# Optimization experiments

Hardware: AMD Instinct MI355X
Metric: run time of the kernel (lower is better)

The kernel has to match this reference:

```python
import jax, jax.numpy as jnp
import numpy as np

V, H, B, T = 32000, 1024, 32, 256  # vocab, rnn_size, batch, seq_length


def setup_inputs() -> dict:
    key = jax.random.key(0)
    ks = jax.random.split(key, 6)
    s = 1.0 / np.sqrt(H)
    return {
        "input_data": jax.random.randint(ks[0], (B, T), 0, V, dtype=jnp.int32),
        "targets": jax.random.randint(ks[1], (B, T), 0, V, dtype=jnp.int32),
        "embedding": jax.random.uniform(ks[2], (V, H), minval=-1.0, maxval=1.0, dtype=jnp.float32),
        "softmax_b": jnp.zeros((V,), jnp.float32),
        "W0": (jax.random.normal(ks[3], (2 * H, 4 * H)) * s).astype(jnp.float32),
        "b0": jnp.zeros((4 * H,), jnp.float32),
        "W1": (jax.random.normal(ks[4], (2 * H, 4 * H)) * s).astype(jnp.float32),
        "b1": jnp.zeros((4 * H,), jnp.float32),
    }


def _lstm_step(x, c, h, W, b):
    # TF LSTMCell: gates i, j, f, o; forget_bias = 1.0
    z = jnp.concatenate([x, h], axis=-1) @ W + b  # [B, 4H]
    i, j, f, o = jnp.split(z, 4, axis=-1)
    c2 = c * jax.nn.sigmoid(f + 1.0) + jax.nn.sigmoid(i) * jnp.tanh(j)
    h2 = jax.nn.sigmoid(o) * jnp.tanh(c2)
    return c2, h2


def reference(input_data, targets, embedding, softmax_b, W0, b0, W1, b1):
    x = embedding[input_data]  # [B, T, H]
    Bb, Hh = x.shape[0], embedding.shape[1]
    zeros = jnp.zeros((Bb, Hh), x.dtype)
    init = ((zeros, zeros), (zeros, zeros))  # ((c0,h0),(c1,h1))

    def step(carry, xt):
        (c0, h0), (c1, h1) = carry
        c0, h0 = _lstm_step(xt, c0, h0, W0, b0)
        c1, h1 = _lstm_step(h0, c1, h1, W1, b1)
        return ((c0, h0), (c1, h1)), h1

    _, outs = jax.lax.scan(step, init, jnp.swapaxes(x, 0, 1))  # [T, B, H]
    output = jnp.swapaxes(outs, 0, 1).reshape(-1, Hh)  # [B*T, H]
    logits = output @ embedding.T + softmax_b  # tied softmax weights, [B*T, V]
    labels = targets.reshape(-1)
    logp = jax.nn.log_softmax(logits)
    loss = -jnp.take_along_axis(logp, labels[:, None], axis=1)[:, 0]
    cost = jnp.sum(loss) / Bb
    return logits, cost
```

## Files before the change

kernel.cpp:

```cpp
#include <hip/hip_runtime.h>
#include <hip/hip_bf16.h>

#define DEV static __device__ __forceinline__

typedef unsigned short u16;
typedef unsigned long long u64;
typedef __attribute__((ext_vector_type(8))) short short8;
typedef __attribute__((ext_vector_type(4))) float f32x4;

constexpr int V = 32000, H = 1024, B = 32, T = 256;
constexpr int BT = B * T;
constexpr int G  = 4 * H;
constexpr int NCH = V / 256;
constexpr int NWG2 = 256;
constexpr int RSTRIDE = 32 * 2048 + 2048;

constexpr size_t SZ_WT    = (size_t)G * 2048 * 2;
constexpr size_t OFF_W0T  = 0;
constexpr size_t OFF_W1T  = OFF_W0T + SZ_WT;
constexpr size_t OFF_EBF  = OFF_W1T + SZ_WT;
constexpr size_t OFF_XBF  = OFF_EBF + (size_t)V * H * 2;
constexpr size_t OFF_XP0  = OFF_XBF + (size_t)BT * H * 2;
constexpr size_t OFF_H1   = OFF_XP0 + (size_t)BT * G * 2;
constexpr size_t OFF_HSEQ = OFF_H1 + (size_t)BT * H * 2;
constexpr size_t SZ_HSEQ  = (size_t)(T + 2) * RSTRIDE * 2;
constexpr size_t OFF_SYNC = OFF_HSEQ + SZ_HSEQ;
constexpr size_t OFF_PMAX = OFF_SYNC + 8192;
constexpr size_t OFF_PSUM = OFF_PMAX + (size_t)BT * NCH * 4;
constexpr size_t OFF_LOSS = OFF_PSUM + (size_t)BT * NCH * 4;

DEV u16 f2bf(float x) {
  union { float f; unsigned int u; } v; v.f = x;
  unsigned int r = v.u + 0x7fffu + ((v.u >> 16) & 1u);
  return (u16)(r >> 16);
}
DEV float bf2f(u16 b) {
  union { unsigned int u; float f; } v; v.u = ((unsigned int)b) << 16;
  return v.f;
}
DEV float sigm(float x) { return 1.f / (1.f + expf(-x)); }

DEV void gload_lds16(const u16* g, u16* l) {
  __builtin_amdgcn_global_load_lds(
      (__attribute__((address_space(1))) void*)g,
      (__attribute__((address_space(3))) void*)l, 16, 0, 0);
}


__global__ void k_transpose_cvt2(const float* __restrict__ in0, u16* __restrict__ out0,
                                 const float* __restrict__ in1, u16* __restrict__ out1) {
  const float* in = blockIdx.z ? in1 : in0;
  u16* out = blockIdx.z ? out1 : out0;
  __shared__ float tile[32][33];
  int bc = blockIdx.x * 32, br = blockIdx.y * 32;
  int tx = threadIdx.x & 31, ty0 = threadIdx.x >> 5;
#pragma unroll
  for (int i = 0; i < 4; ++i) {
    int ty = ty0 + i * 8;
    tile[ty][tx] = in[(size_t)(br + ty) * G + bc + tx];
  }
  __syncthreads();
#pragma unroll
  for (int i = 0; i < 4; ++i) {
    int ty = ty0 + i * 8;
    out[(size_t)(bc + ty) * 2048 + br + tx] = f2bf(tile[tx][ty]);
  }
}

__global__ void k_cvt_bf16(const float* __restrict__ in, u16* __restrict__ out, int n4) {
  int i = blockIdx.x * blockDim.x + threadIdx.x;
  int stride = gridDim.x * blockDim.x;
  for (; i < n4; i += stride) {
    float4 v = ((const float4*)in)[i];
    ushort4 o;
    o.x = f2bf(v.x); o.y = f2bf(v.y); o.z = f2bf(v.z); o.w = f2bf(v.w);
    ((ushort4*)out)[i] = o;
  }
}

__global__ void k_gather_x(const float* __restrict__ emb, const int* __restrict__ inp,
                           u16* __restrict__ Xbf) {
  int row = blockIdx.x;
  int t = row >> 5, b = row & 31;
  int tok = inp[b * T + t];
  const float4* src = (const float4*)(emb + (size_t)tok * H);
  ushort4* dst = (ushort4*)(Xbf + (size_t)row * H);
  float4 v = src[threadIdx.x];
  ushort4 o;
  o.x = f2bf(v.x); o.y = f2bf(v.y); o.z = f2bf(v.z); o.w = f2bf(v.w);
  dst[threadIdx.x] = o;
}

__global__ void k_zero(unsigned int* __restrict__ p, int nwords) {
  int i = blockIdx.x * blockDim.x + threadIdx.x;
  int stride = gridDim.x * blockDim.x;
  for (; i < nwords; i += stride) p[i] = 0u;
}

constexpr int GNT = 32;

DEV void stage256(const u16* __restrict__ A, int lda,
                  const u16* __restrict__ Bt, int ldb,
                  int row0, int col0, u16* lds, int t, int h, int tid) {
  int op = h >> 1, hh = h & 1;
  int wid = tid >> 6, lane = tid & 63;
  int r = hh * 128 + wid * 16 + (lane >> 2);
  int k = t * 32 + (((lane & 3) ^ ((lane >> 2) & 3)) << 3);
  const u16* g = (op == 0) ? (A + (size_t)(row0 + r) * lda + k)
                           : (Bt + (size_t)(col0 + r) * ldb + k);
  u16* l = lds + (size_t)((op * 3 + (t % 3)) * 8192 + (hh * 128 + wid * 16) * 32);
  gload_lds16(g, l);
}

template <int MODE>
__global__ __launch_bounds__(512)
void k_gemm256(const u16* __restrict__ A, int lda,
               const u16* __restrict__ Bt, int ldb,
               float* __restrict__ C, int ldc,
               const float* __restrict__ bias,
               float* __restrict__ pmax, float* __restrict__ psum, int nch) {
  __shared__ alignas(16) u16 lds[6 * 8192];

  unsigned nwg = gridDim.x * gridDim.y;
  unsigned flat = blockIdx.y * gridDim.x + blockIdx.x;
  unsigned nf = (flat & 7) * (nwg >> 3) + (flat >> 3);
  int bx = nf % gridDim.x, by = nf / gridDim.x;
  int row0 = by * 256, col0 = bx * 256;

  int tid = threadIdx.x, lane = tid & 63, wid = tid >> 6;
  int wr = wid >> 2, wc = wid & 3;
  int c15 = lane & 15, q4 = lane >> 4;
  int usw = (q4 ^ (c15 & 3)) << 3;

  f32x4 acc[8][4];
#pragma unroll
  for (int m = 0; m < 8; ++m)
#pragma unroll
    for (int n = 0; n < 4; ++n) acc[m][n] = (f32x4){0.f, 0.f, 0.f, 0.f};

#pragma unroll
  for (int h = 0; h < 4; ++h) stage256(A, lda, Bt, ldb, row0, col0, lds, 0, h, tid);
#pragma unroll
  for (int h = 0; h < 4; ++h) stage256(A, lda, Bt, ldb, row0, col0, lds, 1, h, tid);
  asm volatile("s_waitcnt vmcnt(4)" ::: "memory");
  __builtin_amdgcn_sched_barrier(0);
  __builtin_amdgcn_s_barrier();

  short8 af[4], bfr[4];

  for (int t = 0; t < GNT; ++t) {
    const u16* la = lds + (size_t)(t % 3) * 8192;
    const u16* lb = lds + (size_t)(3 + t % 3) * 8192;

#pragma unroll
    for (int m = 0; m < 4; ++m)
      af[m] = *(const short8*)(la + (wr * 128 + m * 16 + c15) * 32 + usw);
#pragma unroll
    for (int n = 0; n < 4; ++n)
      bfr[n] = *(const short8*)(lb + (wc * 64 + n * 16 + c15) * 32 + usw);
    if (t + 2 < GNT) {
      stage256(A, lda, Bt, ldb, row0, col0, lds, t + 2, 0, tid);
      stage256(A, lda, Bt, ldb, row0, col0, lds, t + 2, 1, tid);
    }
    __builtin_amdgcn_s_barrier();
    asm volatile("s_waitcnt lgkmcnt(0)" ::: "memory");
    __builtin_amdgcn_sched_barrier(0);
    __builtin_amdgcn_s_setprio(1);
#pragma unroll
    for (int m = 0; m < 4; ++m)
#pragma unroll
      for (int n = 0; n < 4; ++n)
        acc[m][n] = __builtin_amdgcn_mfma_f32_16x16x32_bf16(af[m], bfr[n], acc[m][n], 0, 0, 0);
    __builtin_amdgcn_s_setprio(0);
    __builtin_amdgcn_s_barrier();

#pragma unroll
    for (int m = 0; m < 4; ++m)
      af[m] = *(const short8*)(la + (wr * 128 + (m + 4) * 16 + c15) * 32 + usw);
    if (t + 2 < GNT) {
      stage256(A, lda, Bt, ldb, row0, col0, lds, t + 2, 2, tid);
      stage256(A, lda, Bt, ldb, row0, col0, lds, t + 2, 3, tid);
    }
    __builtin_amdgcn_s_barrier();
    asm volatile("s_waitcnt lgkmcnt(0)" ::: "memory");
    __builtin_amdgcn_sched_barrier(0);
    __builtin_amdgcn_s_setprio(1);
#pragma unroll
    for (int m = 0; m < 4; ++m)
#pragma unroll
      for (int n = 0; n < 4; ++n)
        acc[m + 4][n] = __builtin_amdgcn_mfma_f32_16x16x32_bf16(af[m], bfr[n], acc[m + 4][n], 0, 0, 0);
    __builtin_amdgcn_s_setprio(0);
    if (t < GNT - 2) {
      asm volatile("s_waitcnt vmcnt(4)" ::: "memory");
      __builtin_amdgcn_sched_barrier(0);
    } else if (t == GNT - 2) {
      asm volatile("s_waitcnt vmcnt(0)" ::: "memory");
      __builtin_amdgcn_sched_barrier(0);
    }
    __builtin_amdgcn_s_barrier();
  }

  float bias_n[4];
#pragma unroll
  for (int n = 0; n < 4; ++n) bias_n[n] = bias[col0 + wc * 64 + n * 16 + c15];

  float2* red = (float2*)lds;
  __syncthreads();

#pragma unroll
  for (int m = 0; m < 8; ++m) {
#pragma unroll
    for (int jr = 0; jr < 4; ++jr) {
      int rloc = wr * 128 + m * 16 + q4 * 4 + jr;
      int r_g = row0 + rloc;
      float v[4];
#pragma unroll
      for (int n = 0; n < 4; ++n) {
        int c_g = col0 + wc * 64 + n * 16 + c15;
        float val = acc[m][n][jr] + bias_n[n];
        if (MODE == 1) {
          C[(size_t)r_g * ldc + c_g] = val;
        } else {
          int tt = r_g >> 5, bb = r_g & 31;
          int q = c_g >> 10, wgup = (c_g & 1023) >> 3, uu = c_g & 7;
          ((u16*)C)[((((size_t)tt * 128 + wgup) * 32 + bb) * 32) + q * 8 + uu] = f2bf(val);
        }
        v[n] = val;
      }
      if (MODE == 1) {
        float mx = fmaxf(fmaxf(v[0], v[1]), fmaxf(v[2], v[3]));
        float s = __expf(v[0] - mx) + __expf(v[1] - mx) + __expf(v[2] - mx) + __expf(v[3] - mx);
#pragma unroll
        for (int d = 1; d < 16; d <<= 1) {
          float mo = __shfl_xor(mx, d, 64);
          float so = __shfl_xor(s, d, 64);
          float M2 = fmaxf(mx, mo);
          s = s * __expf(mx - M2) + so * __expf(mo - M2);
          mx = M2;
        }
        if (c15 == 0) red[rloc * 4 + wc] = make_float2(mx, s);
      }
    }
  }
  if (MODE == 1) {
    __syncthreads();
    if (tid < 256) {
      float M = -1e30f, S = 0.f;
#pragma unroll
      for (int i = 0; i < 4; ++i) {
        float2 a = red[tid * 4 + i];
        float M2 = fmaxf(M, a.x);
        S = S * __expf(M - M2) + a.y * __expf(a.x - M2);
        M = M2;
      }
      pmax[(size_t)(row0 + tid) * nch + bx] = M;
      psum[(size_t)(row0 + tid) * nch + bx] = S;
    }
  }
}


#define RED(w_, bt_, nt_, r_, c_) red[((((w_)*2 + (bt_)) * 2 + (nt_)) * 16 + (r_)) * 16 + (c_)]

DEV void grid_barrier(int* __restrict__ sync, int wg, int gen) {
  __syncthreads();
  if (threadIdx.x == 0) {
    int g = wg >> 4;
    int old = __hip_atomic_fetch_add(sync + g * 64, 1,
                                     __ATOMIC_RELAXED, __HIP_MEMORY_SCOPE_AGENT);
    if (old == 16 * gen - 1) {
      int m = __hip_atomic_fetch_add(sync + 16 * 64, 1,
                                     __ATOMIC_RELAXED, __HIP_MEMORY_SCOPE_AGENT);
      if (m == 16 * gen - 1)
        __hip_atomic_store(sync + 17 * 64, gen,
                           __ATOMIC_RELAXED, __HIP_MEMORY_SCOPE_AGENT);
    }
    while (__hip_atomic_load(sync + 17 * 64,
                             __ATOMIC_RELAXED, __HIP_MEMORY_SCOPE_AGENT) < gen)
      __builtin_amdgcn_s_sleep(2);
  }
  __builtin_amdgcn_sched_barrier(0);
  __syncthreads();
}

template <int KH, bool IS_L0>
DEV void lstm_role(const u16* __restrict__ WT,
                   const u16* __restrict__ xp0p,
                   const float* __restrict__ zb1,
                   u16* __restrict__ hseq, u16* __restrict__ H1bf,
                   int* __restrict__ sync,
                   float* __restrict__ red, int wgu, int wg) {
  constexpr int KOFF = IS_L0 ? 1024 : 0;
  constexpr int KS = KH / 4;
  constexpr int NKC = KS / 32;
  int tid = threadIdx.x, lane = tid & 63, w = tid >> 6;
  int c15 = lane & 15, q4 = lane >> 4;
  int eb = tid >> 3, eu = tid & 7;

  short8 wfr[2][NKC];
#pragma unroll
  for (int nt = 0; nt < 2; ++nt) {
    int lr = nt * 16 + c15;
    const u16* rp = WT + (size_t)((lr >> 3) * 1024 + wgu * 8 + (lr & 7)) * 2048
                    + KOFF + w * KS + q4 * 8;
#pragma unroll
    for (int kc = 0; kc < NKC; ++kc)
      wfr[nt][kc] = *(const short8*)(rp + kc * 32);
  }

  float zpc[4];
  if (!IS_L0) {
#pragma unroll
    for (int q = 0; q < 4; ++q) zpc[q] = zb1[q * 1024 + wgu * 8 + eu];
  }
  float creg = 0.f;

  for (int tick = 0; tick <= T; ++tick) {
    if (IS_L0 ? (tick < T) : (tick >= 1)) {
      int t = tick;
      float zp[4];
      if (IS_L0) {
#pragma unroll
        for (int q = 0; q < 4; ++q)
          zp[q] = bf2f(xp0p[((((size_t)t * 128 + wgu) * 32 + eb) * 32) + q * 8 + eu]);
      } else {
#pragma unroll
        for (int q = 0; q < 4; ++q) zp[q] = zpc[q];
      }

      const u16* hread = hseq + (size_t)t * RSTRIDE;
      f32x4 acc[2][2];
#pragma unroll
      for (int bt = 0; bt < 2; ++bt)
#pragma unroll
        for (int nt = 0; nt < 2; ++nt) acc[bt][nt] = (f32x4){0.f, 0.f, 0.f, 0.f};

#pragma unroll
      for (int kc = 0; kc < NKC; ++kc) {
        int kh = w * KS + kc * 32 + q4 * 8;
        short8 a0 = *(const short8*)(hread + (size_t)c15 * 2048 + kh);
        short8 a1 = *(const short8*)(hread + (size_t)(16 + c15) * 2048 + kh);
        acc[0][0] = __builtin_amdgcn_mfma_f32_16x16x32_bf16(a0, wfr[0][kc], acc[0][0], 0, 0, 0);
        acc[0][1] = __builtin_amdgcn_mfma_f32_16x16x32_bf16(a0, wfr[1][kc], acc[0][1], 0, 0, 0);
        acc[1][0] = __builtin_amdgcn_mfma_f32_16x16x32_bf16(a1, wfr[0][kc], acc[1][0], 0, 0, 0);
        acc[1][1] = __builtin_amdgcn_mfma_f32_16x16x32_bf16(a1, wfr[1][kc], acc[1][1], 0, 0, 0);
      }

#pragma unroll
      for (int bt = 0; bt < 2; ++bt)
#pragma unroll
        for (int nt = 0; nt < 2; ++nt)
#pragma unroll
          for (int jr = 0; jr < 4; ++jr)
            RED(w, bt, nt, q4 * 4 + jr, c15) = acc[bt][nt][jr];
      __syncthreads();

      int bt = eb >> 4, rr = eb & 15;
      float z[4];
#pragma unroll
      for (int q = 0; q < 4; ++q) {
        int lr = q * 8 + eu, nt = lr >> 4, cc = lr & 15;
        z[q] = RED(0, bt, nt, rr, cc) + RED(1, bt, nt, rr, cc) +
               RED(2, bt, nt, rr, cc) + RED(3, bt, nt, rr, cc) + zp[q];
      }
      float gi = sigm(z[0]);
      float gj = tanhf(z[1]);
      float gf = sigm(z[2] + 1.f);
      float go = sigm(z[3]);
      creg = creg * gf + gi * gj;
      float hv = go * tanhf(creg);

      int hb = (int)f2bf(hv);
      int hp = __shfl_xor(hb, 1, 64);
      if (!(tid & 1)) {
        unsigned int pack = (unsigned int)(u16)hb | ((unsigned int)(u16)hp << 16);
        u16* hwr = hseq + (size_t)(t + 1) * RSTRIDE + (IS_L0 ? 0 : 1024);
        __hip_atomic_store((unsigned int*)(hwr + (size_t)eb * 2048 + wgu * 8 + eu), pack,
                           __ATOMIC_RELAXED, __HIP_MEMORY_SCOPE_AGENT);
        if (!IS_L0)
          *(unsigned int*)(H1bf + ((size_t)eb * T + (t - 1)) * H + wgu * 8 + eu) = pack;
      }
    }
    grid_barrier(sync, wg, tick + 1);
  }
}

__global__ __launch_bounds__(256, 1)
void k_lstm_persistent(const u16* __restrict__ W0T, const u16* __restrict__ W1T,
                       const u16* __restrict__ xp0p, const float* __restrict__ b1,
                       u16* __restrict__ hseq, u16* __restrict__ H1bf,
                       int* __restrict__ sync) {
  __shared__ float red[4 * 2 * 2 * 16 * 16];
  int wg = blockIdx.x;
  if (wg < 128)
    lstm_role<1024, true>(W0T, xp0p, nullptr, hseq, H1bf, sync, red, wg, wg);
  else
    lstm_role<2048, false>(W1T, nullptr, b1, hseq, H1bf, sync, red, wg - 128, wg);
}

__global__ void k_rowfin(const float* __restrict__ pmax, const float* __restrict__ psum,
                         const float* __restrict__ Cl, const int* __restrict__ targets,
                         float* __restrict__ loss) {
  int lane = threadIdx.x & 63, wv = threadIdx.x >> 6;
  int row = blockIdx.x * 4 + wv;
  float mx = -1e30f, s = 0.f;
  if (lane < NCH) { mx = pmax[(size_t)row * NCH + lane]; s = psum[(size_t)row * NCH + lane]; }
  if (lane + 64 < NCH) {
    float m2 = pmax[(size_t)row * NCH + 64 + lane];
    float s2 = psum[(size_t)row * NCH + 64 + lane];
    float M2 = fmaxf(mx, m2);
    s = s * __expf(mx - M2) + s2 * __expf(m2 - M2);
    mx = M2;
  }
#pragma unroll
  for (int d = 1; d < 64; d <<= 1) {
    float mo = __shfl_xor(mx, d, 64);
    float so = __shfl_xor(s, d, 64);
    float M2 = fmaxf(mx, mo);
    s = s * __expf(mx - M2) + so * __expf(mo - M2);
    mx = M2;
  }
  if (lane == 0) {
    float logZ = mx + logf(s);
    int tgt = targets[row];
    float xt = Cl[(size_t)row * V + tgt];
    loss[row] = logZ - xt;
  }
}

__global__ void k_cost(const float* __restrict__ loss, float* __restrict__ out) {
  int tid = threadIdx.x, lane = tid & 63, w = tid >> 6;
  float s = 0.f;
  for (int i = tid; i < BT; i += 256) s += loss[i];
#pragma unroll
  for (int d = 1; d < 64; d <<= 1) s += __shfl_xor(s, d, 64);
  __shared__ float ws4[4];
  if (lane == 0) ws4[w] = s;
  __syncthreads();
  if (tid == 0) out[0] = (ws4[0] + ws4[1] + ws4[2] + ws4[3]) * (1.0f / B);
}

extern "C" void kernel_launch(void* const* d_in, const int* in_sizes, int n_in,
                              void* d_out, int out_size, void* d_ws, size_t ws_size,
                              hipStream_t stream) {
  const int*   input_data = (const int*)d_in[0];
  const int*   targets    = (const int*)d_in[1];
  const float* emb        = (const float*)d_in[2];
  const float* softmax_b  = (const float*)d_in[3];
  const float* W0         = (const float*)d_in[4];
  const float* b0         = (const float*)d_in[5];
  const float* W1         = (const float*)d_in[6];
  const float* b1         = (const float*)d_in[7];
  float* out = (float*)d_out;
  char*  ws  = (char*)d_ws;

  u16*   W0T  = (u16*)(ws + OFF_W0T);
  u16*   W1T  = (u16*)(ws + OFF_W1T);
  u16*   Ebf  = (u16*)(ws + OFF_EBF);
  u16*   Xbf  = (u16*)(ws + OFF_XBF);
  u16*   xp0p = (u16*)(ws + OFF_XP0);
  u16*   H1bf = (u16*)(ws + OFF_H1);
  u16*   hseq = (u16*)(ws + OFF_HSEQ);
  int*   sync = (int*)(ws + OFF_SYNC);
  float* pmax = (float*)(ws + OFF_PMAX);
  float* psum = (float*)(ws + OFF_PSUM);
  float* lossb= (float*)(ws + OFF_LOSS);

  k_transpose_cvt2<<<dim3(G / 32, 2048 / 32, 2), 256, 0, stream>>>(W0, W0T, W1, W1T);
  k_cvt_bf16<<<2048, 256, 0, stream>>>(emb, Ebf, V * H / 4);
  k_gather_x<<<BT, 256, 0, stream>>>(emb, input_data, Xbf);
  k_zero<<<64, 256, 0, stream>>>((unsigned int*)(ws + OFF_HSEQ), RSTRIDE);
  k_zero<<<1, 256, 0, stream>>>((unsigned int*)(ws + OFF_SYNC), 2048);

  k_gemm256<0><<<dim3(G / 256, BT / 256), 512, 0, stream>>>(
      Xbf, H, W0T, 2048, (float*)xp0p, 0, b0, nullptr, nullptr, 0);

  k_lstm_persistent<<<dim3(NWG2), dim3(256), 0, stream>>>(
      W0T, W1T, xp0p, b1, hseq, H1bf, sync);

  k_gemm256<1><<<dim3(V / 256, BT / 256), 512, 0, stream>>>(
      H1bf, H, Ebf, H, out, V, softmax_b, pmax, psum, NCH);

  k_rowfin<<<BT / 4, 256, 0, stream>>>(pmax, psum, out, targets, lossb);
  k_cost<<<1, 256, 0, stream>>>(lossb, out + (size_t)BT * V);
}
```

Before: 2.743 ms.

## Fuse vocab GEMM into persistent LSTM kernel using idle waves between barriers

The persistent LSTM kernel now runs 512 threads per workgroup. Four waves do the recurrence, and the other four compute 32x64 tiles of the output-logits GEMM for timesteps whose layer-1 hidden states are already published, working in bounded quanta between grid barriers. This is meant to hide the large vocab GEMM behind the latency-bound recurrence and remove the separate GEMM launch. The cost is smaller, less efficient GEMM tiles with more partial-softmax chunks (NCH grows from V/256 to V/64), H1 stored in time-major order, and the pmax buffer aliased over the gather buffer. Contention could slow the recurrence's critical path.

```diff
diff --git a/kernel.cpp b/kernel.cpp
--- a/kernel.cpp
+++ b/kernel.cpp
@@ -11,7 +11,7 @@
 constexpr int V = 32000, H = 1024, B = 32, T = 256;
 constexpr int BT = B * T;
 constexpr int G  = 4 * H;
-constexpr int NCH = V / 256;
+constexpr int NCH = V / 64;
 constexpr int NWG2 = 256;
 constexpr int RSTRIDE = 32 * 2048 + 2048;
 
@@ -25,8 +25,8 @@
 constexpr size_t OFF_HSEQ = OFF_H1 + (size_t)BT * H * 2;
 constexpr size_t SZ_HSEQ  = (size_t)(T + 2) * RSTRIDE * 2;
 constexpr size_t OFF_SYNC = OFF_HSEQ + SZ_HSEQ;
-constexpr size_t OFF_PMAX = OFF_SYNC + 8192;
-constexpr size_t OFF_PSUM = OFF_PMAX + (size_t)BT * NCH * 4;
+constexpr size_t OFF_PMAX = OFF_XBF;
+constexpr size_t OFF_PSUM = OFF_SYNC + 8192;
 constexpr size_t OFF_LOSS = OFF_PSUM + (size_t)BT * NCH * 4;
 
 DEV u16 f2bf(float x) {
@@ -112,13 +112,11 @@
   gload_lds16(g, l);
 }
 
-template <int MODE>
 __global__ __launch_bounds__(512)
 void k_gemm256(const u16* __restrict__ A, int lda,
                const u16* __restrict__ Bt, int ldb,
                float* __restrict__ C, int ldc,
-               const float* __restrict__ bias,
-               float* __restrict__ pmax, float* __restrict__ psum, int nch) {
+               const float* __restrict__ bias) {
   __shared__ alignas(16) u16 lds[6 * 8192];
 
   unsigned nwg = gridDim.x * gridDim.y;
@@ -205,57 +203,19 @@
 #pragma unroll
   for (int n = 0; n < 4; ++n) bias_n[n] = bias[col0 + wc * 64 + n * 16 + c15];
 
-  float2* red = (float2*)lds;
-  __syncthreads();
-
 #pragma unroll
   for (int m = 0; m < 8; ++m) {
 #pragma unroll
     for (int jr = 0; jr < 4; ++jr) {
-      int rloc = wr * 128 + m * 16 + q4 * 4 + jr;
-      int r_g = row0 + rloc;
-      float v[4];
+      int r_g = row0 + wr * 128 + m * 16 + q4 * 4 + jr;
 #pragma unroll
       for (int n = 0; n < 4; ++n) {
         int c_g = col0 + wc * 64 + n * 16 + c15;
         float val = acc[m][n][jr] + bias_n[n];
-        if (MODE == 1) {
-          C[(size_t)r_g * ldc + c_g] = val;
-        } else {
-          int tt = r_g >> 5, bb = r_g & 31;
-          int q = c_g >> 10, wgup = (c_g & 1023) >> 3, uu = c_g & 7;
-          ((u16*)C)[((((size_t)tt * 128 + wgup) * 32 + bb) * 32) + q * 8 + uu] = f2bf(val);
-        }
-        v[n] = val;
-      }
-      if (MODE == 1) {
-        float mx = fmaxf(fmaxf(v[0], v[1]), fmaxf(v[2], v[3]));
-        float s = __expf(v[0] - mx) + __expf(v[1] - mx) + __expf(v[2] - mx) + __expf(v[3] - mx);
-#pragma unroll
-        for (int d = 1; d < 16; d <<= 1) {
-          float mo = __shfl_xor(mx, d, 64);
-          float so = __shfl_xor(s, d, 64);
-          float M2 = fmaxf(mx, mo);
-          s = s * __expf(mx - M2) + so * __expf(mo - M2);
-          mx = M2;
-        }
-        if (c15 == 0) red[rloc * 4 + wc] = make_float2(mx, s);
-      }
-    }
-  }
-  if (MODE == 1) {
-    __syncthreads();
-    if (tid < 256) {
-      float M = -1e30f, S = 0.f;
-#pragma unroll
-      for (int i = 0; i < 4; ++i) {
-        float2 a = red[tid * 4 + i];
-        float M2 = fmaxf(M, a.x);
-        S = S * __expf(M - M2) + a.y * __expf(a.x - M2);
-        M = M2;
-      }
-      pmax[(size_t)(row0 + tid) * nch + bx] = M;
-      psum[(size_t)(row0 + tid) * nch + bx] = S;
+        int tt = r_g >> 5, bb = r_g & 31;
+        int q = c_g >> 10, wgup = (c_g & 1023) >> 3, uu = c_g & 7;
+        ((u16*)C)[((((size_t)tt * 128 + wgup) * 32 + bb) * 32) + q * 8 + uu] = f2bf(val);
+      }
     }
   }
 }
@@ -263,61 +223,153 @@
 
 #define RED(w_, bt_, nt_, r_, c_) red[((((w_)*2 + (bt_)) * 2 + (nt_)) * 16 + (r_)) * 16 + (c_)]
 
-DEV void grid_barrier(int* __restrict__ sync, int wg, int gen) {
-  __syncthreads();
-  if (threadIdx.x == 0) {
-    int g = wg >> 4;
-    int old = __hip_atomic_fetch_add(sync + g * 64, 1,
-                                     __ATOMIC_RELAXED, __HIP_MEMORY_SCOPE_AGENT);
-    if (old == 16 * gen - 1) {
-      int m = __hip_atomic_fetch_add(sync + 16 * 64, 1,
-                                     __ATOMIC_RELAXED, __HIP_MEMORY_SCOPE_AGENT);
-      if (m == 16 * gen - 1)
-        __hip_atomic_store(sync + 17 * 64, gen,
-                           __ATOMIC_RELAXED, __HIP_MEMORY_SCOPE_AGENT);
-    }
-    while (__hip_atomic_load(sync + 17 * 64,
-                             __ATOMIC_RELAXED, __HIP_MEMORY_SCOPE_AGENT) < gen)
-      __builtin_amdgcn_s_sleep(2);
-  }
-  __builtin_amdgcn_sched_barrier(0);
-  __syncthreads();
+DEV void g32_stage(const u16* __restrict__ H1, const u16* __restrict__ Eb,
+                   int row0, int col0, int s, u16* slice, int lane) {
+  int ksw = s * 32 + (((lane & 3) ^ ((lane >> 2) & 3)) << 3);
+  const u16* ga = H1 + (size_t)(row0 + (lane >> 2)) * 1024 + ksw;
+  const u16* gb = Eb + (size_t)(col0 + (lane >> 2)) * 1024 + ksw;
+  u16* aw = slice + (s & 1) * 1024;
+  u16* bw = slice + 2048 + (s & 1) * 2048;
+#pragma unroll
+  for (int g = 0; g < 2; ++g) gload_lds16(ga + g * 16 * 1024, aw + g * 512);
+#pragma unroll
+  for (int g = 0; g < 4; ++g) gload_lds16(gb + g * 16 * 1024, bw + g * 512);
+}
+
+DEV void g32_step(const u16* slice, int s, int c15, int q4, f32x4 (&acc)[2][4]) {
+  const u16* la = slice + (s & 1) * 1024;
+  const u16* lb = slice + 2048 + (s & 1) * 2048;
+  int usw = (q4 ^ (c15 & 3)) << 3;
+  short8 af[2], bf8[4];
+#pragma unroll
+  for (int m = 0; m < 2; ++m) af[m] = *(const short8*)(la + (m * 16 + c15) * 32 + usw);
+#pragma unroll
+  for (int n = 0; n < 4; ++n) bf8[n] = *(const short8*)(lb + (n * 16 + c15) * 32 + usw);
+#pragma unroll
+  for (int m = 0; m < 2; ++m)
+#pragma unroll
+    for (int n = 0; n < 4; ++n)
+      acc[m][n] = __builtin_amdgcn_mfma_f32_16x16x32_bf16(af[m], bf8[n], acc[m][n], 0, 0, 0);
+}
+
+DEV void g32_epi(f32x4 (&acc)[2][4], int row0, int col0, int nx,
+                 float* __restrict__ Cl, const float* __restrict__ smb,
+                 float* __restrict__ pmax, float* __restrict__ psum,
+                 int c15, int q4) {
+  float bias_n[4];
+#pragma unroll
+  for (int n = 0; n < 4; ++n) bias_n[n] = smb[col0 + n * 16 + c15];
+#pragma unroll
+  for (int m = 0; m < 2; ++m) {
+#pragma unroll
+    for (int jr = 0; jr < 4; ++jr) {
+      int r_g = row0 + m * 16 + q4 * 4 + jr;
+      float v[4];
+#pragma unroll
+      for (int n = 0; n < 4; ++n) {
+        v[n] = acc[m][n][jr] + bias_n[n];
+        Cl[(size_t)r_g * V + col0 + n * 16 + c15] = v[n];
+      }
+      float mx = fmaxf(fmaxf(v[0], v[1]), fmaxf(v[2], v[3]));
+      float sm = __expf(v[0] - mx) + __expf(v[1] - mx) + __expf(v[2] - mx) + __expf(v[3] - mx);
+#pragma unroll
+      for (int d = 1; d < 16; d <<= 1) {
+        float mo = __shfl_xor(mx, d, 64);
+        float so = __shfl_xor(sm, d, 64);
+        float M2 = fmaxf(mx, mo);
+        sm = sm * __expf(mx - M2) + so * __expf(mo - M2);
+        mx = M2;
+      }
+      if (c15 == 0) {
+        pmax[(size_t)r_g * NCH + nx] = mx;
+        psum[(size_t)r_g * NCH + nx] = sm;
+      }
+    }
+  }
+}
+
+DEV void g32_quantum(int rel, int budget, int& gj, int& gs, bool& gstaged,
+                     f32x4 (&acc)[2][4], int nx, int gp,
+                     const u16* __restrict__ H1, const u16* __restrict__ Eb,
+                     float* __restrict__ Cl, const float* __restrict__ smb,
+                     float* __restrict__ pmax, float* __restrict__ psum,
+                     u16* slice, int lane, int c15, int q4) {
+  while (budget > 0 && gj < 128) {
+    int t = 2 * gj + gp;
+    if (gs == 0) {
+      if (rel < t + 2) break;
+#pragma unroll
+      for (int m = 0; m < 2; ++m)
+#pragma unroll
+        for (int n = 0; n < 4; ++n) acc[m][n] = (f32x4){0.f, 0.f, 0.f, 0.f};
+    }
+    int row0 = t * 32, col0 = nx * 64;
+    if (!gstaged) g32_stage(H1, Eb, row0, col0, gs, slice, lane);
+    if (gs + 1 < 32) {
+      g32_stage(H1, Eb, row0, col0, gs + 1, slice, lane);
+      asm volatile("s_waitcnt vmcnt(6)" ::: "memory");
+      gstaged = true;
+    } else {
+      asm volatile("s_waitcnt vmcnt(0)" ::: "memory");
+      gstaged = false;
+    }
+    g32_step(slice, gs, c15, q4, acc);
+    ++gs; --budget;
+    if (gs == 32) {
+      g32_epi(acc, row0, col0, nx, Cl, smb, pmax, psum, c15, q4);
+      ++gj; gs = 0; gstaged = false;
+    }
+  }
 }
 
 template <int KH, bool IS_L0>
-DEV void lstm_role(const u16* __restrict__ WT,
-                   const u16* __restrict__ xp0p,
-                   const float* __restrict__ zb1,
-                   u16* __restrict__ hseq, u16* __restrict__ H1bf,
-                   int* __restrict__ sync,
-                   float* __restrict__ red, int wgu, int wg) {
+DEV void fused_role(const u16* __restrict__ WT, const u16* __restrict__ xp0p,
+                    const float* __restrict__ zb1,
+                    u16* __restrict__ hseq, u16* __restrict__ H1bf,
+                    int* __restrict__ sync,
+                    const u16* __restrict__ Ebf, float* __restrict__ Cl,
+                    const float* __restrict__ smb,
+                    float* __restrict__ pmax, float* __restrict__ psum,
+                    float* __restrict__ red, u16* __restrict__ glds,
+                    int wgu, int wg) {
   constexpr int KOFF = IS_L0 ? 1024 : 0;
   constexpr int KS = KH / 4;
   constexpr int NKC = KS / 32;
-  int tid = threadIdx.x, lane = tid & 63, w = tid >> 6;
+  int tid = threadIdx.x, lane = tid & 63, wid = tid >> 6;
   int c15 = lane & 15, q4 = lane >> 4;
   int eb = tid >> 3, eu = tid & 7;
+  bool isL = wid < 4;
 
   short8 wfr[2][NKC];
-#pragma unroll
-  for (int nt = 0; nt < 2; ++nt) {
-    int lr = nt * 16 + c15;
-    const u16* rp = WT + (size_t)((lr >> 3) * 1024 + wgu * 8 + (lr & 7)) * 2048
-                    + KOFF + w * KS + q4 * 8;
-#pragma unroll
-    for (int kc = 0; kc < NKC; ++kc)
-      wfr[nt][kc] = *(const short8*)(rp + kc * 32);
-  }
-
   float zpc[4];
-  if (!IS_L0) {
-#pragma unroll
-    for (int q = 0; q < 4; ++q) zpc[q] = zb1[q * 1024 + wgu * 8 + eu];
-  }
   float creg = 0.f;
+  if (isL) {
+#pragma unroll
+    for (int nt = 0; nt < 2; ++nt) {
+      int lr = nt * 16 + c15;
+      const u16* rp = WT + (size_t)((lr >> 3) * 1024 + wgu * 8 + (lr & 7)) * 2048
+                      + KOFF + wid * KS + q4 * 8;
+#pragma unroll
+      for (int kc = 0; kc < NKC; ++kc)
+        wfr[nt][kc] = *(const short8*)(rp + kc * 32);
+    }
+    if (!IS_L0) {
+#pragma unroll
+      for (int q = 0; q < 4; ++q) zpc[q] = zb1[q * 1024 + wgu * 8 + eu];
+    }
+  }
+
+  int wgl = wg * 4 + (wid - 4);
+  bool gact = (!isL) && (wgl < 1000);
+  int nx = wgl >> 1, gp = wgl & 1;
+  int gj = 0, gs = 0;
+  bool gstaged = false;
+  f32x4 gacc[2][4];
+  u16* slice = glds + (size_t)(wid & 3) * 6144;
 
   for (int tick = 0; tick <= T; ++tick) {
-    if (IS_L0 ? (tick < T) : (tick >= 1)) {
+    bool act = IS_L0 ? (tick < T) : (tick >= 1);
+    if (isL && act) {
       int t = tick;
       float zp[4];
       if (IS_L0) {
@@ -338,7 +390,7 @@
 
 #pragma unroll
       for (int kc = 0; kc < NKC; ++kc) {
-        int kh = w * KS + kc * 32 + q4 * 8;
+        int kh = wid * KS + kc * 32 + q4 * 8;
         short8 a0 = *(const short8*)(hread + (size_t)c15 * 2048 + kh);
         short8 a1 = *(const short8*)(hread + (size_t)(16 + c15) * 2048 + kh);
         acc[0][0] = __builtin_amdgcn_mfma_f32_16x16x32_bf16(a0, wfr[0][kc], acc[0][0], 0, 0, 0);
@@ -346,16 +398,27 @@
         acc[1][0] = __builtin_amdgcn_mfma_f32_16x16x32_bf16(a1, wfr[0][kc], acc[1][0], 0, 0, 0);
         acc[1][1] = __builtin_amdgcn_mfma_f32_16x16x32_bf16(a1, wfr[1][kc], acc[1][1], 0, 0, 0);
       }
-
 #pragma unroll
       for (int bt = 0; bt < 2; ++bt)
 #pragma unroll
         for (int nt = 0; nt < 2; ++nt)
 #pragma unroll
           for (int jr = 0; jr < 4; ++jr)
-            RED(w, bt, nt, q4 * 4 + jr, c15) = acc[bt][nt][jr];
-      __syncthreads();
-
+            RED(wid, bt, nt, q4 * 4 + jr, c15) = acc[bt][nt][jr];
+    }
+    __syncthreads();
+
+    if (isL && act) {
+      int t = tick;
+      float zp[4];
+      if (IS_L0) {
+#pragma unroll
+        for (int q = 0; q < 4; ++q)
+          zp[q] = bf2f(xp0p[((((size_t)t * 128 + wgu) * 32 + eb) * 32) + q * 8 + eu]);
+      } else {
+#pragma unroll
+        for (int q = 0; q < 4; ++q) zp[q] = zpc[q];
+      }
       int bt = eb >> 4, rr = eb & 15;
       float z[4];
 #pragma unroll
@@ -365,10 +428,10 @@
                RED(2, bt, nt, rr, cc) + RED(3, bt, nt, rr, cc) + zp[q];
       }
       float gi = sigm(z[0]);
-      float gj = tanhf(z[1]);
+      float gj2 = tanhf(z[1]);
       float gf = sigm(z[2] + 1.f);
       float go = sigm(z[3]);
-      creg = creg * gf + gi * gj;
+      creg = creg * gf + gi * gj2;
       float hv = go * tanhf(creg);
 
       int hb = (int)f2bf(hv);
@@ -379,24 +442,61 @@
         __hip_atomic_store((unsigned int*)(hwr + (size_t)eb * 2048 + wgu * 8 + eu), pack,
                            __ATOMIC_RELAXED, __HIP_MEMORY_SCOPE_AGENT);
         if (!IS_L0)
-          *(unsigned int*)(H1bf + ((size_t)eb * T + (t - 1)) * H + wgu * 8 + eu) = pack;
-      }
-    }
-    grid_barrier(sync, wg, tick + 1);
-  }
-}
-
-__global__ __launch_bounds__(256, 1)
-void k_lstm_persistent(const u16* __restrict__ W0T, const u16* __restrict__ W1T,
-                       const u16* __restrict__ xp0p, const float* __restrict__ b1,
-                       u16* __restrict__ hseq, u16* __restrict__ H1bf,
-                       int* __restrict__ sync) {
+          __hip_atomic_store(
+              (unsigned int*)(H1bf + ((size_t)(t - 1) * 32 + eb) * H + wgu * 8 + eu), pack,
+              __ATOMIC_RELAXED, __HIP_MEMORY_SCOPE_AGENT);
+      }
+    }
+    __syncthreads();
+
+    if (tid == 0) {
+      int g = wg >> 4;
+      int gen = tick + 1;
+      int old = __hip_atomic_fetch_add(sync + g * 64, 1,
+                                       __ATOMIC_RELAXED, __HIP_MEMORY_SCOPE_AGENT);
+      if (old == 16 * gen - 1) {
+        int m = __hip_atomic_fetch_add(sync + 16 * 64, 1,
+                                       __ATOMIC_RELAXED, __HIP_MEMORY_SCOPE_AGENT);
+        if (m == 16 * gen - 1)
+          __hip_atomic_store(sync + 17 * 64, gen,
+                             __ATOMIC_RELAXED, __HIP_MEMORY_SCOPE_AGENT);
+      }
+      while (__hip_atomic_load(sync + 17 * 64,
+                               __ATOMIC_RELAXED, __HIP_MEMORY_SCOPE_AGENT) < gen)
+        __builtin_amdgcn_s_sleep(2);
+    } else if (gact) {
+      int rv = __hip_atomic_load(sync + 17 * 64,
+                                 __ATOMIC_RELAXED, __HIP_MEMORY_SCOPE_AGENT);
+      int rel = __builtin_amdgcn_readfirstlane(rv);
+      g32_quantum(rel, 18, gj, gs, gstaged, gacc, nx, gp,
+                  H1bf, Ebf, Cl, smb, pmax, psum, slice, lane, c15, q4);
+    }
+    __builtin_amdgcn_sched_barrier(0);
+    __syncthreads();
+  }
+
+  if (gact)
+    g32_quantum(T + 1, 1 << 28, gj, gs, gstaged, gacc, nx, gp,
+                H1bf, Ebf, Cl, smb, pmax, psum, slice, lane, c15, q4);
+}
+
+__global__ __launch_bounds__(512, 1)
+void k_lstm_fused(const u16* __restrict__ W0T, const u16* __restrict__ W1T,
+                  const u16* __restrict__ xp0p, const float* __restrict__ b1,
+                  u16* __restrict__ hseq, u16* __restrict__ H1bf,
+                  int* __restrict__ sync,
+                  const u16* __restrict__ Ebf, float* __restrict__ Cl,
+                  const float* __restrict__ smb,
+                  float* __restrict__ pmax, float* __restrict__ psum) {
   __shared__ float red[4 * 2 * 2 * 16 * 16];
+  __shared__ alignas(16) u16 glds[4 * 6144];
   int wg = blockIdx.x;
   if (wg < 128)
-    lstm_role<1024, true>(W0T, xp0p, nullptr, hseq, H1bf, sync, red, wg, wg);
+    fused_role<1024, true>(W0T, xp0p, nullptr, hseq, H1bf, sync,
+                           Ebf, Cl, smb, pmax, psum, red, glds, wg, wg);
   else
-    lstm_role<2048, false>(W1T, nullptr, b1, hseq, H1bf, sync, red, wg - 128, wg);
+    fused_role<2048, false>(W1T, nullptr, b1, hseq, H1bf, sync,
+                            Ebf, Cl, smb, pmax, psum, red, glds, wg - 128, wg);
 }
 
 __global__ void k_rowfin(const float* __restrict__ pmax, const float* __restrict__ psum,
@@ -405,10 +505,9 @@
   int lane = threadIdx.x & 63, wv = threadIdx.x >> 6;
   int row = blockIdx.x * 4 + wv;
   float mx = -1e30f, s = 0.f;
-  if (lane < NCH) { mx = pmax[(size_t)row * NCH + lane]; s = psum[(size_t)row * NCH + lane]; }
-  if (lane + 64 < NCH) {
-    float m2 = pmax[(size_t)row * NCH + 64 + lane];
-    float s2 = psum[(size_t)row * NCH + 64 + lane];
+  for (int i = lane; i < NCH; i += 64) {
+    float m2 = pmax[(size_t)row * NCH + i];
+    float s2 = psum[(size_t)row * NCH + i];
     float M2 = fmaxf(mx, m2);
     s = s * __expf(mx - M2) + s2 * __expf(m2 - M2);
     mx = M2;
@@ -473,14 +572,11 @@
   k_zero<<<64, 256, 0, stream>>>((unsigned int*)(ws + OFF_HSEQ), RSTRIDE);
   k_zero<<<1, 256, 0, stream>>>((unsigned int*)(ws + OFF_SYNC), 2048);
 
-  k_gemm256<0><<<dim3(G / 256, BT / 256), 512, 0, stream>>>(
-      Xbf, H, W0T, 2048, (float*)xp0p, 0, b0, nullptr, nullptr, 0);
-
-  k_lstm_persistent<<<dim3(NWG2), dim3(256), 0, stream>>>(
-      W0T, W1T, xp0p, b1, hseq, H1bf, sync);
-
-  k_gemm256<1><<<dim3(V / 256, BT / 256), 512, 0, stream>>>(
-      H1bf, H, Ebf, H, out, V, softmax_b, pmax, psum, NCH);
+  k_gemm256<<<dim3(G / 256, BT / 256), 512, 0, stream>>>(
+      Xbf, H, W0T, 2048, (float*)xp0p, 0, b0);
+
+  k_lstm_fused<<<dim3(NWG2), dim3(512), 0, stream>>>(
+      W0T, W1T, xp0p, b1, hseq, H1bf, sync, Ebf, out, softmax_b, pmax, psum);
 
   k_rowfin<<<BT / 4, 256, 0, stream>>>(pmax, psum, out, targets, lossb);
   k_cost<<<1, 256, 0, stream>>>(lossb, out + (size_t)BT * V);
```

Result: slower. 6.165 ms (+124.8%).
